# Kernel optimization log

Measured on AMD Instinct MI355X. Metric: run time of the kernel, lower is better.

The kernel has to match this reference:

```python
import jax, jax.numpy as jnp
import numpy as np
import math

NX = 1024
N_HEAD = 16
HEAD_DIM = NX // N_HEAD
N_CTX = 2048
REL_VOCAB = 64
B = 2
S = 2048


def setup_inputs() -> dict:
    key = jax.random.key(0)
    ks = jax.random.split(key, 7)
    x = jax.random.normal(ks[0], (B, S, NX), dtype=jnp.float32)
    rel = jax.random.randint(ks[1], (B, S, S), 0, REL_VOCAB, dtype=jnp.int64)
    sc = 0.02
    Wqkv = jax.random.normal(ks[2], (NX, 3 * NX), dtype=jnp.float32) * sc
    bqkv = jnp.zeros((3 * NX,), dtype=jnp.float32)
    Wproj = jax.random.normal(ks[3], (NX, NX), dtype=jnp.float32) * sc
    bproj = jnp.zeros((NX,), dtype=jnp.float32)
    rel_emb = jax.random.normal(ks[4], (REL_VOCAB, N_HEAD), dtype=jnp.float32) * sc
    return {"x": x, "Wqkv": Wqkv, "bqkv": bqkv, "Wproj": Wproj,
            "bproj": bproj, "rel_emb": rel_emb, "rel": rel}


def reference(x, Wqkv, bqkv, Wproj, bproj, rel_emb, rel):
    Bsz, Sq, _ = x.shape
    qkv = x @ Wqkv + bqkv                      # [B,S,3*nx]
    q, k, v = jnp.split(qkv, 3, axis=-1)
    def split_heads(t):                        # [B,S,nx] -> [B,H,S,D]
        return t.reshape(Bsz, Sq, N_HEAD, HEAD_DIM).transpose(0, 2, 1, 3)
    q, k, v = split_heads(q), split_heads(k), split_heads(v)
    w = jnp.einsum('bhqd,bhkd->bhqk', q, k) / math.sqrt(HEAD_DIM)
    bmask = jnp.tril(jnp.ones((Sq, Sq), dtype=w.dtype))[None, None]  # [1,1,S,S]
    w = w * bmask - 1e10 * (1.0 - bmask)
    relw = rel_emb[rel].transpose(0, 3, 1, 2)  # [B,S,S,H] -> [B,H,S,S]
    w = w * (relw * bmask)                     # faithful: masked scores become 0
    p = jax.nn.softmax(w, axis=-1)
    a = jnp.einsum('bhqk,bhkd->bhqd', p, v)
    a = a.transpose(0, 2, 1, 3).reshape(Bsz, Sq, NX)  # merge heads
    return a @ Wproj + bproj
```

## Files before the change

kernel.cpp:

```cpp
#include <hip/hip_runtime.h>

typedef unsigned short u16;
typedef unsigned char u8;
typedef __attribute__((ext_vector_type(8))) short short8;
typedef __attribute__((ext_vector_type(4))) short short4v;
typedef __attribute__((ext_vector_type(4))) float f32x4;

#define GLD16(g, l) __builtin_amdgcn_global_load_lds( \
    (const __attribute__((address_space(1))) void*)(g), \
    (__attribute__((address_space(3))) void*)(l), 16, 0, 0)

__device__ __forceinline__ float bf2f(u16 u){
  union { unsigned int i; float f; } v; v.i = ((unsigned int)u) << 16; return v.f;
}
__device__ __forceinline__ u16 f2bf(float f){
  union { float f; unsigned int i; } v; v.f = f;
  unsigned int u = v.i;
  unsigned int r = (u + 0x7FFFu + ((u >> 16) & 1u)) >> 16;
  return (u16)r;
}

__device__ __forceinline__ f32x4 mfma16(short4v a, short4v b, f32x4 c){
#if __has_builtin(__builtin_amdgcn_mfma_f32_16x16x16bf16_1k)
  return __builtin_amdgcn_mfma_f32_16x16x16bf16_1k(a, b, c, 0, 0, 0);
#else
  asm volatile("s_nop 1\n\tv_mfma_f32_16x16x16_bf16 %0, %1, %2, %0" : "+v"(c) : "v"(a), "v"(b));
  return c;
#endif
}

__global__ __launch_bounds__(256) void prep_k(const float* __restrict__ x, u16* __restrict__ xb,
                                              const float* __restrict__ Wqkv, u16* __restrict__ wqkvT,
                                              const float* __restrict__ Wproj, u16* __restrict__ wprojT,
                                              const int* __restrict__ rel, u8* __restrict__ rel8){
  const int bid = blockIdx.x, t = threadIdx.x;
  if (bid < 4096){
    int i = bid * 256 + t;
    float4 v = ((const float4*)x)[i];
    unsigned long long pk = (unsigned long long)f2bf(v.x)
      | ((unsigned long long)f2bf(v.y) << 16)
      | ((unsigned long long)f2bf(v.z) << 32)
      | ((unsigned long long)f2bf(v.w) << 48);
    ((unsigned long long*)xb)[i] = pk;
  } else if (bid < 8192){
    const float* W; u16* Wt; int K, N, blk, nbx;
    if (bid < 7168){ W = Wqkv; Wt = wqkvT; K = 1024; N = 3072; blk = bid - 4096; nbx = 96; }
    else           { W = Wproj; Wt = wprojT; K = 1024; N = 1024; blk = bid - 7168; nbx = 32; }
    __shared__ float tl[32][33];
    int n0 = (blk % nbx) * 32, k0 = (blk / nbx) * 32;
    int tx = t & 31, ty = t >> 5;
    for (int i = ty; i < 32; i += 8)
      tl[i][tx] = W[(size_t)(k0 + i) * N + n0 + tx];
    __syncthreads();
    for (int i = ty; i < 32; i += 8)
      Wt[(size_t)(n0 + i) * K + k0 + tx] = f2bf(tl[tx][i]);
  } else {
    int i = (bid - 8192) * 256 + t;
    int4 v = ((const int4*)rel)[i];
    unsigned int pk = (unsigned int)(v.x & 255) | ((unsigned int)(v.y & 255) << 8)
      | ((unsigned int)(v.z & 255) << 16) | ((unsigned int)(v.w & 255) << 24);
    ((unsigned int*)rel8)[i] = pk;
  }
}

template<int BN, int MODE>
__global__ __launch_bounds__(256) void gemm_bt_k(const u16* __restrict__ A, const u16* __restrict__ Bt,
                                                 const float* __restrict__ bias,
                                                 u16* __restrict__ oq, u16* __restrict__ okk, u16* __restrict__ ov,
                                                 float* __restrict__ of,
                                                 int M, int N, int K){
  __shared__ u16 la[128 * 64];
  __shared__ u16 lb[BN * 64];
  const int t = threadIdx.x, w = t >> 6, lane = t & 63;
  const int l15 = lane & 15, l4 = lane >> 4;
  const int m0 = blockIdx.y * 128, n0 = blockIdx.x * BN;
  const int wr = w >> 1, wc = w & 1;
  constexpr int NI = BN / 32;
  f32x4 acc[4][NI] = {};
  const u16* Abase = A + (size_t)m0 * K;
  const u16* Bbase = Bt + (size_t)n0 * K;
  for (int kt = 0; kt < K; kt += 64){
    __syncthreads();
#pragma unroll
    for (int i = 0; i < 4; ++i){
      int chunk = i * 256 + t;
      int row = chunk >> 3, cs = chunk & 7;
      int c = cs ^ (row & 7);
      GLD16(Abase + (size_t)row * K + kt + c * 8, &la[(i * 256 + w * 64) * 8]);
    }
#pragma unroll
    for (int i = 0; i < BN / 32; ++i){
      int chunk = i * 256 + t;
      int row = chunk >> 3, cs = chunk & 7;
      int c = cs ^ (row & 7);
      GLD16(Bbase + (size_t)row * K + kt + c * 8, &lb[(i * 256 + w * 64) * 8]);
    }
    asm volatile("s_waitcnt vmcnt(0)" ::: "memory");
    __syncthreads();
    short8 af[4][2], bfr[NI][2];
#pragma unroll
    for (int mi = 0; mi < 4; ++mi){
      int row = wr * 64 + mi * 16 + l15;
#pragma unroll
      for (int h = 0; h < 2; ++h)
        af[mi][h] = *(const short8*)&la[row * 64 + (((h * 4 + l4) ^ (row & 7)) * 8)];
    }
#pragma unroll
    for (int ni = 0; ni < NI; ++ni){
      int row = wc * (BN / 2) + ni * 16 + l15;
#pragma unroll
      for (int h = 0; h < 2; ++h)
        bfr[ni][h] = *(const short8*)&lb[row * 64 + (((h * 4 + l4) ^ (row & 7)) * 8)];
    }
#pragma unroll
    for (int mi = 0; mi < 4; ++mi)
#pragma unroll
      for (int ni = 0; ni < NI; ++ni){
        acc[mi][ni] = __builtin_amdgcn_mfma_f32_16x16x32_bf16(af[mi][0], bfr[ni][0], acc[mi][ni], 0, 0, 0);
        acc[mi][ni] = __builtin_amdgcn_mfma_f32_16x16x32_bf16(af[mi][1], bfr[ni][1], acc[mi][ni], 0, 0, 0);
      }
  }
#pragma unroll
  for (int mi = 0; mi < 4; ++mi){
#pragma unroll
    for (int ni = 0; ni < NI; ++ni){
#pragma unroll
      for (int r = 0; r < 4; ++r){
        int m = m0 + wr * 64 + mi * 16 + l4 * 4 + r;
        int n = n0 + wc * (BN / 2) + ni * 16 + l15;
        float v = acc[mi][ni][r] + bias[n];
        if (MODE == 0){
          int tt = n >> 10, rr = n & 1023, head = rr >> 6, d = rr & 63;
          int b = m >> 11, s = m & 2047;
          u16* dst = (tt == 0) ? oq : (tt == 1) ? okk : ov;
          dst[(((size_t)(b * 16 + head)) * 2048 + s) * 64 + d] = f2bf(v);
        } else {
          of[(size_t)m * N + n] = v;
        }
      }
    }
  }
}

__global__ __launch_bounds__(256) void transpose_v_k(const u16* __restrict__ vb, u16* __restrict__ vt,
                                                     float* __restrict__ vpart){
  __shared__ u16 tl[64][65];
  int bh = blockIdx.x >> 5, c = blockIdx.x & 31, s0 = c * 64;
  int t = threadIdx.x;
#pragma unroll
  for (int rsub = 0; rsub < 16; ++rsub){
    int idx = rsub * 256 + t;
    int i = idx >> 6, d = idx & 63;
    tl[i][d] = vb[(((size_t)bh * 2048) + s0 + i) * 64 + d];
  }
  __syncthreads();
#pragma unroll
  for (int rsub = 0; rsub < 16; ++rsub){
    int idx = rsub * 256 + t;
    int d = idx >> 6, j = idx & 63;
    int pj = (j & 3) | (((j >> 2) & 3) << 4) | (((j >> 4) & 3) << 2);
    vt[(((size_t)bh * 64) + d) * 2048 + s0 + pj] = tl[j][d];
  }
  if (t < 64){
    float s = 0.f;
#pragma unroll 8
    for (int j = 0; j < 64; ++j) s += bf2f(tl[j][t]);
    vpart[((size_t)bh * 32 + c) * 64 + t] = s;
  }
}

__global__ void vsufscan_k(const float* __restrict__ vpart, float* __restrict__ vsuf){
  int bh = blockIdx.x, d = threadIdx.x;
  float run = 0.f;
  vsuf[((size_t)bh * 33 + 32) * 64 + d] = 0.f;
  for (int c = 31; c >= 0; --c){
    run += vpart[((size_t)bh * 32 + c) * 64 + d];
    vsuf[((size_t)bh * 33 + c) * 64 + d] = run;
  }
}

template<int U8, int SPLIT>
__global__ __launch_bounds__(256, 4) void attn_k(const u16* __restrict__ qb, const u16* __restrict__ kb,
                                                 const u16* __restrict__ vt, const float* __restrict__ vsuf,
                                                 const void* __restrict__ relp, const float* __restrict__ rel_emb,
                                                 u16* __restrict__ ab, float* __restrict__ pacc,
                                                 float* __restrict__ prsum){
  __shared__ u16 Kt[2][64 * 64];
  __shared__ u16 Vt[2][64 * 64];
  __shared__ float remb[64];
  int p, hf, bh;
  if (SPLIT){
    const int lid = blockIdx.x;
    const int bhgrp = lid & 7, within = (lid >> 3) & 3, pf = lid >> 5;
    bh = bhgrp * 4 + within;
    p = pf >> 1; hf = pf & 1;
  } else {
    p = blockIdx.x; hf = 0; bh = blockIdx.y;
  }
  const int b = bh >> 4, h = bh & 15;
  const int TA = p, TB = 31 - p;
  const int q0A = TA * 64, q0B = TB * 64;
  const int tid = threadIdx.x, w = tid >> 6, lane = tid & 63;
  const int l15 = lane & 15, l4 = lane >> 4;
  if (tid < 64) remb[tid] = rel_emb[tid * 16 + h] * (0.125f * 1.44269504088896f);
  const u16* kbh = kb + ((size_t)bh * 2048) * 64;
  const u16* vbh = vt + ((size_t)bh * 64) * 2048;
  const u16* qA = qb + (((size_t)bh * 2048) + q0A + w * 16 + l15) * 64 + l4 * 8;
  const u16* qB = qb + (((size_t)bh * 2048) + q0B + w * 16 + l15) * 64 + l4 * 8;
  const short8 aqA0 = *(const short8*)qA, aqA1 = *(const short8*)(qA + 32);
  const short8 aqB0 = *(const short8*)qB, aqB1 = *(const short8*)(qB + 32);
  const u8*  r8A  = (const u8*)relp + ((size_t)b * 2048 + q0A + w * 16 + l15) * 2048;
  const u8*  r8B  = (const u8*)relp + ((size_t)b * 2048 + q0B + w * 16 + l15) * 2048;
  const int* r32A = (const int*)relp + ((size_t)b * 2048 + q0A + w * 16 + l15) * 2048;
  const int* r32B = (const int*)relp + ((size_t)b * 2048 + q0B + w * 16 + l15) * 2048;

  const int srow0 = (tid >> 3), srow1 = 32 + (tid >> 3);
  const int scs = tid & 7;
  const int sc0 = scs ^ (srow0 & 7), sc1 = scs ^ (srow1 & 7);
  const int sldsoff = (w * 64) * 8;

#define STAGE(ktile, buf) do {                                                       \
    GLD16(kbh + (size_t)((ktile) * 64 + srow0) * 64 + sc0 * 8, &Kt[buf][sldsoff]);   \
    GLD16(kbh + (size_t)((ktile) * 64 + srow1) * 64 + sc1 * 8, &Kt[buf][2048 + sldsoff]); \
    GLD16(vbh + (size_t)srow0 * 2048 + (ktile) * 64 + sc0 * 8, &Vt[buf][sldsoff]);   \
    GLD16(vbh + (size_t)srow1 * 2048 + (ktile) * 64 + sc1 * 8, &Vt[buf][2048 + sldsoff]); \
  } while (0)

  f32x4 acc[4] = {};
  float rsum = 0.f;
  unsigned int relc[4], reln[4];

  auto relload = [&](bool isA, int kt, unsigned int* dst){
    int off = kt * 64 + 4 * l4;
    if (U8){
      const u8* pp = isA ? r8A : r8B;
#pragma unroll
      for (int t = 0; t < 4; ++t) dst[t] = *(const unsigned int*)(pp + off + 16 * t);
    } else {
      const int* pp = isA ? r32A : r32B;
#pragma unroll
      for (int t = 0; t < 4; ++t){
        int4 v4 = *(const int4*)(pp + off + 16 * t);
        dst[t] = (unsigned int)(v4.x & 255) | ((unsigned int)(v4.y & 255) << 8)
               | ((unsigned int)(v4.z & 255) << 16) | ((unsigned int)(v4.w & 255) << 24);
      }
    }
  };

  auto writeout = [&](int Td, int q0){
    asm volatile("s_nop 7\n\ts_nop 7" :::);
    float s = rsum;
    s += __shfl_xor(s, 16);
    s += __shfl_xor(s, 32);
    float invZ = 1.f / (s + (float)(2048 - (Td + 1) * 64));
    int qg = q0 + w * 16 + l15;
    const float* sufp = vsuf + ((size_t)bh * 33 + Td + 1) * 64;
#pragma unroll
    for (int ni = 0; ni < 4; ++ni){
      float4 sv = *(const float4*)(sufp + ni * 16 + 4 * l4);
      unsigned int lo2 = (unsigned int)f2bf((acc[ni][0] + sv.x) * invZ)
                       | ((unsigned int)f2bf((acc[ni][1] + sv.y) * invZ) << 16);
      unsigned int hi2 = (unsigned int)f2bf((acc[ni][2] + sv.z) * invZ)
                       | ((unsigned int)f2bf((acc[ni][3] + sv.w) * invZ) << 16);
      uint2 o; o.x = lo2; o.y = hi2;
      *(uint2*)(ab + ((size_t)b * 2048 + qg) * 1024 + h * 64 + ni * 16 + 4 * l4) = o;
    }
  };

  const int lo = (SPLIT && hf) ? 17 : 0;
  const int hi = (SPLIT && !hf) ? 17 : 33;

  {
    bool isA0 = (lo <= TA);
    int kt0 = isA0 ? lo : lo - TA - 1;
    STAGE(kt0, 0);
    relload(isA0, kt0, relc);
  }
  __syncthreads();

  for (int it = lo; it < hi; ++it){
    const bool isA = (it <= TA);
    const int kt = isA ? it : (it - TA - 1);
    const int cur = (it - lo) & 1;

    if (it + 1 < hi){
      const bool nA = (it + 1 <= TA);
      const int nkt = nA ? (it + 1) : (it - TA);
      STAGE(nkt, cur ^ 1);
      relload(nA, nkt, reln);
    }

    const short8 a0 = isA ? aqA0 : aqB0;
    const short8 a1 = isA ? aqA1 : aqB1;
    const bool diag = (kt == (isA ? TA : TB));

    short4v pk[4];
    __builtin_amdgcn_s_setprio(1);
#pragma unroll
    for (int t = 0; t < 4; ++t){
      const int krow = 16 * t + l15;
      const u16* kbase = &Kt[cur][krow * 64];
      short8 bk0 = *(const short8*)&kbase[((l4)     ^ (krow & 7)) * 8];
      short8 bk1 = *(const short8*)&kbase[((4 + l4) ^ (krow & 7)) * 8];
      f32x4 sf = {0.f, 0.f, 0.f, 0.f};
      sf = __builtin_amdgcn_mfma_f32_16x16x32_bf16(bk0, a0, sf, 0, 0, 0);
      sf = __builtin_amdgcn_mfma_f32_16x16x32_bf16(bk1, a1, sf, 0, 0, 0);
      unsigned int rw = relc[t];
      const int kk = 16 * t + 4 * l4;
      float prv[4];
#pragma unroll
      for (int r = 0; r < 4; ++r){
        float sc = sf[r] * remb[(rw >> (8 * r)) & 255];
        if (diag) sc = (kk + r <= w * 16 + l15) ? sc : 0.f;
        float pv = __builtin_amdgcn_exp2f(sc);
        rsum += pv;
        prv[r] = pv;
      }
      union { unsigned int u[2]; short4v s; } pu;
      asm("v_cvt_pk_bf16_f32 %0, %1, %2" : "=v"(pu.u[0]) : "v"(prv[0]), "v"(prv[1]));
      asm("v_cvt_pk_bf16_f32 %0, %1, %2" : "=v"(pu.u[1]) : "v"(prv[2]), "v"(prv[3]));
      pk[t] = pu.s;
    }
    asm volatile("s_nop 2" :::);
#pragma unroll
    for (int ni = 0; ni < 4; ++ni){
      const int drow = ni * 16 + l15;
      const u16* vbase = &Vt[cur][drow * 64];
      short8 vv0 = *(const short8*)&vbase[(((2 * l4)     ^ (drow & 7))) * 8];
      short8 vv1 = *(const short8*)&vbase[(((2 * l4 + 1) ^ (drow & 7))) * 8];
      short4v va0 = {vv0[0], vv0[1], vv0[2], vv0[3]};
      short4v va1 = {vv0[4], vv0[5], vv0[6], vv0[7]};
      short4v va2 = {vv1[0], vv1[1], vv1[2], vv1[3]};
      short4v va3 = {vv1[4], vv1[5], vv1[6], vv1[7]};
      acc[ni] = mfma16(va0, pk[0], acc[ni]);
      acc[ni] = mfma16(va1, pk[1], acc[ni]);
      acc[ni] = mfma16(va2, pk[2], acc[ni]);
      acc[ni] = mfma16(va3, pk[3], acc[ni]);
    }
    __builtin_amdgcn_s_setprio(0);

    if (it == TA){
      writeout(TA, q0A);
#pragma unroll
      for (int ni = 0; ni < 4; ++ni) acc[ni] = f32x4{0.f, 0.f, 0.f, 0.f};
      rsum = 0.f;
    }
    if (it + 1 < hi){
#pragma unroll
      for (int t = 0; t < 4; ++t) relc[t] = reln[t];
    }
    __syncthreads();
  }
#undef STAGE

  if (SPLIT){
    asm volatile("s_nop 7\n\ts_nop 7" :::);
    float s = rsum;
    s += __shfl_xor(s, 16);
    s += __shfl_xor(s, 32);
    const size_t slot = (((size_t)bh * 16 + p) * 2 + hf);
    float* pslot = pacc + slot * 4096;
#pragma unroll
    for (int ni = 0; ni < 4; ++ni)
      *(f32x4*)(pslot + (w * 16 + l15) * 64 + ni * 16 + 4 * l4) = acc[ni];
    if (l4 == 0) prsum[slot * 64 + w * 16 + l15] = s;
  } else {
    writeout(TB, q0B);
  }
}

__global__ __launch_bounds__(256) void attn_fin_k(const float* __restrict__ pacc,
                                                  const float* __restrict__ prsum,
                                                  const float* __restrict__ vsuf,
                                                  u16* __restrict__ ab){
  const int p = blockIdx.x, bh = blockIdx.y;
  const int b = bh >> 4, h = bh & 15;
  const int TB = 31 - p, q0 = TB * 64;
  const int r = threadIdx.x >> 2, cg = threadIdx.x & 3;
  const size_t slot = ((size_t)bh * 16 + p) * 2;
  const size_t base = slot * 4096 + r * 64 + cg * 16;
  float rs = prsum[slot * 64 + r] + prsum[(slot + 1) * 64 + r];
  float invZ = 1.f / (rs + (float)(2048 - (TB + 1) * 64));
  const float* sufp = vsuf + ((size_t)bh * 33 + TB + 1) * 64 + cg * 16;
  u16 o[16];
#pragma unroll
  for (int j = 0; j < 4; ++j){
    f32x4 a0 = *(const f32x4*)(pacc + base + j * 4);
    f32x4 a1 = *(const f32x4*)(pacc + base + 4096 + j * 4);
    f32x4 sv = *(const f32x4*)(sufp + j * 4);
#pragma unroll
    for (int e = 0; e < 4; ++e) o[j * 4 + e] = f2bf((a0[e] + a1[e] + sv[e]) * invZ);
  }
  u16* dst = ab + ((size_t)b * 2048 + q0 + r) * 1024 + h * 64 + cg * 16;
  *(uint4*)dst = *(const uint4*)&o[0];
  *(uint4*)(dst + 8) = *(const uint4*)&o[8];
}

extern "C" void kernel_launch(void* const* d_in, const int* in_sizes, int n_in,
                              void* d_out, int out_size, void* d_ws, size_t ws_size,
                              hipStream_t stream){
  const float* x       = (const float*)d_in[0];
  const float* Wqkv    = (const float*)d_in[1];
  const float* bqkv    = (const float*)d_in[2];
  const float* Wproj   = (const float*)d_in[3];
  const float* bproj   = (const float*)d_in[4];
  const float* rel_emb = (const float*)d_in[5];
  const int*   rel     = (const int*)d_in[6];
  float* out = (float*)d_out;

  char* ws = (char*)d_ws;
  u16* xb     = (u16*)(ws);
  u16* wqkvT  = (u16*)(ws + (8ull  << 20));
  u16* wprojT = (u16*)(ws + (14ull << 20));
  u16* qb     = (u16*)(ws + (16ull << 20));
  u16* kb     = (u16*)(ws + (24ull << 20));
  u16* vb     = (u16*)(ws + (32ull << 20));
  u16* vtb    = (u16*)(ws + (40ull << 20));
  float* vsuf = (float*)(ws + (48ull << 20));
  float* vpart= (float*)(ws + (48ull << 20) + (512ull << 10));
  float* pacc = (float*)(ws + (49ull << 20));
  float* prsum= (float*)(ws + (65ull << 20) + (512ull << 10));
  u8*   rel8  = (u8*)(ws + (66ull << 20));
  const bool useSplit = ws_size >= (67ull << 20);
  const bool useU8    = ws_size >= (75ull << 20);

  prep_k<<<useU8 ? 16384 : 8192, 256, 0, stream>>>(x, xb, Wqkv, wqkvT, Wproj, wprojT, rel, rel8);
  gemm_bt_k<128, 0><<<dim3(24, 32), 256, 0, stream>>>(xb, wqkvT, bqkv, qb, kb, vb, nullptr, 4096, 3072, 1024);
  transpose_v_k<<<1024, 256, 0, stream>>>(vb, vtb, vpart);
  vsufscan_k<<<32, 64, 0, stream>>>(vpart, vsuf);
  if (useU8)
    attn_k<1, 1><<<dim3(1024), 256, 0, stream>>>(qb, kb, vtb, vsuf, rel8, rel_emb, xb, pacc, prsum);
  else if (useSplit)
    attn_k<0, 1><<<dim3(1024), 256, 0, stream>>>(qb, kb, vtb, vsuf, rel, rel_emb, xb, pacc, prsum);
  else
    attn_k<0, 0><<<dim3(16, 32), 256, 0, stream>>>(qb, kb, vtb, vsuf, rel, rel_emb, xb, pacc, prsum);
  if (useSplit || useU8)
    attn_fin_k<<<dim3(16, 32), 256, 0, stream>>>(pacc, prsum, vsuf, xb);
  gemm_bt_k<64, 1><<<dim3(16, 32), 256, 0, stream>>>(xb, wprojT, bproj, nullptr, nullptr, nullptr, out, 4096, 1024, 1024);
}
```

Measured before the change: 143.6 us.

## Fuse V transpose into QKV GEMM epilogue with triple-buffered pipelined loads

Adds a dedicated QKV GEMM that uses a 3-stage global_load_lds pipeline with K-tile 32, explicit vmcnt waits and MFMA priority raising. Its epilogue writes V directly in the transposed, permuted layout the attention kernel expects. This removes the separate transpose kernel and the extra round trip of V through memory. The V suffix-sum is recomputed from the transposed buffer in a single kernel that does the scan in LDS, so the separate partial-sum and scan kernels go away. The cost is narrower 8-byte V stores and new hand-tuned wait counts that must stay correct.

Measured after the change: 138.9 us. 3.3% less time.

```diff
diff --git a/kernel.cpp b/kernel.cpp
--- a/kernel.cpp
+++ b/kernel.cpp
@@ -63,11 +63,92 @@
   }
 }
 
-template<int BN, int MODE>
+__global__ __launch_bounds__(256) void gemm_qkv_k(const u16* __restrict__ A, const u16* __restrict__ Bt,
+                                                  const float* __restrict__ bias,
+                                                  u16* __restrict__ oq, u16* __restrict__ okk, u16* __restrict__ vt){
+  __shared__ u16 la[3][128 * 32];
+  __shared__ u16 lb[3][128 * 32];
+  const int K = 1024;
+  const int t = threadIdx.x, w = t >> 6, lane = t & 63;
+  const int l15 = lane & 15, l4 = lane >> 4;
+  const int m0 = blockIdx.y * 128, n0 = blockIdx.x * 128;
+  const int wr = w >> 1, wc = w & 1;
+  f32x4 acc[4][4] = {};
+  const u16* Abase = A + (size_t)m0 * K;
+  const u16* Bbase = Bt + (size_t)n0 * K;
+
+  const int srow0 = t >> 2, srow1 = 64 + (t >> 2);
+  const int cg = t & 3;
+  const int sc0 = cg ^ (srow0 & 3), sc1 = cg ^ (srow1 & 3);
+  const int wbase0 = (w * 64) * 8, wbase1 = (256 + w * 64) * 8;
+
+#define QSTAGE(kt, buf) do {                                                        \
+    GLD16(Abase + (size_t)srow0 * K + (kt) * 32 + sc0 * 8, &la[buf][wbase0]);       \
+    GLD16(Abase + (size_t)srow1 * K + (kt) * 32 + sc1 * 8, &la[buf][wbase1]);       \
+    GLD16(Bbase + (size_t)srow0 * K + (kt) * 32 + sc0 * 8, &lb[buf][wbase0]);       \
+    GLD16(Bbase + (size_t)srow1 * K + (kt) * 32 + sc1 * 8, &lb[buf][wbase1]);       \
+  } while (0)
+
+  QSTAGE(0, 0);
+  QSTAGE(1, 1);
+  for (int ki = 0; ki < 32; ++ki){
+    __builtin_amdgcn_sched_barrier(0);
+    if (ki < 31) asm volatile("s_waitcnt vmcnt(4)" ::: "memory");
+    else         asm volatile("s_waitcnt vmcnt(0)" ::: "memory");
+    __builtin_amdgcn_s_barrier();
+    __builtin_amdgcn_sched_barrier(0);
+    if (ki + 2 < 32) QSTAGE(ki + 2, (ki + 2) % 3);
+    const int cb = ki % 3;
+    short8 af[4], bfr[4];
+#pragma unroll
+    for (int mi = 0; mi < 4; ++mi){
+      int row = wr * 64 + mi * 16 + l15;
+      af[mi] = *(const short8*)&la[cb][row * 32 + ((l4 ^ (row & 3)) * 8)];
+    }
+#pragma unroll
+    for (int ni = 0; ni < 4; ++ni){
+      int row = wc * 64 + ni * 16 + l15;
+      bfr[ni] = *(const short8*)&lb[cb][row * 32 + ((l4 ^ (row & 3)) * 8)];
+    }
+    __builtin_amdgcn_s_setprio(1);
+#pragma unroll
+    for (int mi = 0; mi < 4; ++mi)
+#pragma unroll
+      for (int ni = 0; ni < 4; ++ni)
+        acc[mi][ni] = __builtin_amdgcn_mfma_f32_16x16x32_bf16(af[mi], bfr[ni], acc[mi][ni], 0, 0, 0);
+    __builtin_amdgcn_s_setprio(0);
+  }
+#undef QSTAGE
+
+#pragma unroll
+  for (int mi = 0; mi < 4; ++mi){
+    const int m_base = m0 + wr * 64 + mi * 16 + l4 * 4;
+    const int bsel = m_base >> 11, s0q = m_base & 2047;
+#pragma unroll
+    for (int ni = 0; ni < 4; ++ni){
+      int n = n0 + wc * 64 + ni * 16 + l15;
+      float vb = bias[n];
+      int tt = n >> 10, rr = n & 1023, head = rr >> 6, dd = rr & 63;
+      if (tt == 2){
+        int c = s0q >> 6, w6 = s0q & 63;
+        int pj0 = (((w6 >> 2) & 3) << 4) | (((w6 >> 4) & 3) << 2);
+        u16 o4[4];
+#pragma unroll
+        for (int r = 0; r < 4; ++r) o4[r] = f2bf(acc[mi][ni][r] + vb);
+        *(uint2*)(vt + ((size_t)(bsel * 16 + head) * 64 + dd) * 2048 + c * 64 + pj0) = *(const uint2*)o4;
+      } else {
+        u16* dst = (tt == 0) ? oq : okk;
+#pragma unroll
+        for (int r = 0; r < 4; ++r)
+          dst[(((size_t)(bsel * 16 + head)) * 2048 + s0q + r) * 64 + dd] = f2bf(acc[mi][ni][r] + vb);
+      }
+    }
+  }
+}
+
+template<int BN>
 __global__ __launch_bounds__(256) void gemm_bt_k(const u16* __restrict__ A, const u16* __restrict__ Bt,
-                                                 const float* __restrict__ bias,
-                                                 u16* __restrict__ oq, u16* __restrict__ okk, u16* __restrict__ ov,
-                                                 float* __restrict__ of,
+                                                 const float* __restrict__ bias, float* __restrict__ of,
                                                  int M, int N, int K){
   __shared__ u16 la[128 * 64];
   __shared__ u16 lb[BN * 64];
@@ -128,54 +209,35 @@
       for (int r = 0; r < 4; ++r){
         int m = m0 + wr * 64 + mi * 16 + l4 * 4 + r;
         int n = n0 + wc * (BN / 2) + ni * 16 + l15;
-        float v = acc[mi][ni][r] + bias[n];
-        if (MODE == 0){
-          int tt = n >> 10, rr = n & 1023, head = rr >> 6, d = rr & 63;
-          int b = m >> 11, s = m & 2047;
-          u16* dst = (tt == 0) ? oq : (tt == 1) ? okk : ov;
-          dst[(((size_t)(b * 16 + head)) * 2048 + s) * 64 + d] = f2bf(v);
-        } else {
-          of[(size_t)m * N + n] = v;
-        }
+        of[(size_t)m * N + n] = acc[mi][ni][r] + bias[n];
       }
     }
   }
 }
 
-__global__ __launch_bounds__(256) void transpose_v_k(const u16* __restrict__ vb, u16* __restrict__ vt,
-                                                     float* __restrict__ vpart){
-  __shared__ u16 tl[64][65];
-  int bh = blockIdx.x >> 5, c = blockIdx.x & 31, s0 = c * 64;
-  int t = threadIdx.x;
-#pragma unroll
-  for (int rsub = 0; rsub < 16; ++rsub){
-    int idx = rsub * 256 + t;
-    int i = idx >> 6, d = idx & 63;
-    tl[i][d] = vb[(((size_t)bh * 2048) + s0 + i) * 64 + d];
+__global__ __launch_bounds__(256) void vsuf2_k(const u16* __restrict__ vt, float* __restrict__ vsuf){
+  __shared__ float part[32][64];
+  const int bh = blockIdx.x;
+  const int d = threadIdx.x & 63, qtr = threadIdx.x >> 6;
+  const u16* row = vt + ((size_t)bh * 64 + d) * 2048;
+  for (int c = qtr * 8; c < qtr * 8 + 8; ++c){
+    float s = 0.f;
+#pragma unroll
+    for (int jv = 0; jv < 8; ++jv){
+      short8 v = *(const short8*)(row + c * 64 + jv * 8);
+#pragma unroll
+      for (int e = 0; e < 8; ++e) s += bf2f((u16)v[e]);
+    }
+    part[c][d] = s;
   }
   __syncthreads();
-#pragma unroll
-  for (int rsub = 0; rsub < 16; ++rsub){
-    int idx = rsub * 256 + t;
-    int d = idx >> 6, j = idx & 63;
-    int pj = (j & 3) | (((j >> 2) & 3) << 4) | (((j >> 4) & 3) << 2);
-    vt[(((size_t)bh * 64) + d) * 2048 + s0 + pj] = tl[j][d];
-  }
-  if (t < 64){
-    float s = 0.f;
-#pragma unroll 8
-    for (int j = 0; j < 64; ++j) s += bf2f(tl[j][t]);
-    vpart[((size_t)bh * 32 + c) * 64 + t] = s;
-  }
-}
-
-__global__ void vsufscan_k(const float* __restrict__ vpart, float* __restrict__ vsuf){
-  int bh = blockIdx.x, d = threadIdx.x;
-  float run = 0.f;
-  vsuf[((size_t)bh * 33 + 32) * 64 + d] = 0.f;
-  for (int c = 31; c >= 0; --c){
-    run += vpart[((size_t)bh * 32 + c) * 64 + d];
-    vsuf[((size_t)bh * 33 + c) * 64 + d] = run;
+  if (threadIdx.x < 64){
+    float run = 0.f;
+    vsuf[((size_t)bh * 33 + 32) * 64 + d] = 0.f;
+    for (int c = 31; c >= 0; --c){
+      run += part[c][d];
+      vsuf[((size_t)bh * 33 + c) * 64 + d] = run;
+    }
   }
 }
 
@@ -414,10 +476,8 @@
   u16* wprojT = (u16*)(ws + (14ull << 20));
   u16* qb     = (u16*)(ws + (16ull << 20));
   u16* kb     = (u16*)(ws + (24ull << 20));
-  u16* vb     = (u16*)(ws + (32ull << 20));
   u16* vtb    = (u16*)(ws + (40ull << 20));
   float* vsuf = (float*)(ws + (48ull << 20));
-  float* vpart= (float*)(ws + (48ull << 20) + (512ull << 10));
   float* pacc = (float*)(ws + (49ull << 20));
   float* prsum= (float*)(ws + (65ull << 20) + (512ull << 10));
   u8*   rel8  = (u8*)(ws + (66ull << 20));
@@ -425,9 +485,8 @@
   const bool useU8    = ws_size >= (75ull << 20);
 
   prep_k<<<useU8 ? 16384 : 8192, 256, 0, stream>>>(x, xb, Wqkv, wqkvT, Wproj, wprojT, rel, rel8);
-  gemm_bt_k<128, 0><<<dim3(24, 32), 256, 0, stream>>>(xb, wqkvT, bqkv, qb, kb, vb, nullptr, 4096, 3072, 1024);
-  transpose_v_k<<<1024, 256, 0, stream>>>(vb, vtb, vpart);
-  vsufscan_k<<<32, 64, 0, stream>>>(vpart, vsuf);
+  gemm_qkv_k<<<dim3(24, 32), 256, 0, stream>>>(xb, wqkvT, bqkv, qb, kb, vtb);
+  vsuf2_k<<<32, 256, 0, stream>>>(vtb, vsuf);
   if (useU8)
     attn_k<1, 1><<<dim3(1024), 256, 0, stream>>>(qb, kb, vtb, vsuf, rel8, rel_emb, xb, pacc, prsum);
   else if (useSplit)
@@ -436,5 +495,5 @@
     attn_k<0, 0><<<dim3(16, 32), 256, 0, stream>>>(qb, kb, vtb, vsuf, rel, rel_emb, xb, pacc, prsum);
   if (useSplit || useU8)
     attn_fin_k<<<dim3(16, 32), 256, 0, stream>>>(pacc, prsum, vsuf, xb);
-  gemm_bt_k<64, 1><<<dim3(16, 32), 256, 0, stream>>>(xb, wprojT, bproj, nullptr, nullptr, nullptr, out, 4096, 1024, 1024);
-}
+  gemm_bt_k<64><<<dim3(16, 32), 256, 0, stream>>>(xb, wprojT, bproj, out, 4096, 1024, 1024);
+}
```
